# Kernel optimization log

Measured on AMD Instinct MI355X. Metric: run time of the kernel, lower is better.

Reference implementation:

```python
import jax, jax.numpy as jnp
import numpy as np

FFT_SIZE = 16384

def setup_inputs() -> dict:
    key = jax.random.key(0)
    k1, k2 = jax.random.split(key)
    u = jax.random.normal(k1, (8, 1024, 8192), dtype=jnp.float32)
    k = jax.random.normal(k2, (1024, 8192), dtype=jnp.float32)
    return {"u": u, "k": k}

def reference(u, k):
    # Faithful port of PyTorchFFTConv.forward with fft_size=FFT_SIZE.
    L = u.shape[-1]
    u_f32 = u.astype(jnp.float32)
    k_f32 = k.astype(jnp.float32)
    if k_f32.ndim == 2:
        k_f32 = k_f32[None]  # (1, H, L) -> broadcasts over batch
    u_fft = jnp.fft.rfft(u_f32, n=FFT_SIZE, axis=-1)   # (B, H, fft/2+1) complex64
    k_fft = jnp.fft.rfft(k_f32, n=FFT_SIZE, axis=-1)
    y_fft = u_fft * k_fft / FFT_SIZE
    # irfft with norm='forward' (no 1/n on inverse) combined with the /fft_s above
    # yields the standard circular convolution, matching the torch code exactly.
    y = jnp.fft.irfft(y_fft, n=FFT_SIZE, axis=-1, norm='forward')
    return y[..., :L].astype(jnp.float32)
```

## Files before the change

### kernel.cpp

```cpp
#include <hip/hip_runtime.h>

#define NFFT 16384
#define LSIG 8192
#define NH   1024
#define NTH  512
#define LDSC (NFFT + ((NFFT >> 5) << 1))

__device__ __forceinline__ int PADC(int i) { return i + ((i >> 5) << 1); }
__device__ __forceinline__ int PADI(int i) { return i + (i >> 5); }

struct cplx { float x, y; };
__device__ __forceinline__ cplx cadd(cplx a, cplx b){ return {a.x+b.x, a.y+b.y}; }
__device__ __forceinline__ cplx csub(cplx a, cplx b){ return {a.x-b.x, a.y-b.y}; }
__device__ __forceinline__ cplx cmul(cplx a, cplx b){ return {a.x*b.x - a.y*b.y, a.x*b.y + a.y*b.x}; }

template<int V> struct ic { static constexpr int value = V; };
template<int Start, int End, typename F>
__device__ __forceinline__ void cfor(F&& f) {
  if constexpr (Start < End) { f(ic<Start>{}); cfor<Start+1, End>(static_cast<F&&>(f)); }
}

constexpr float W32C32[32] = {
  1.0f, 0.9807852804f, 0.9238795325f, 0.8314696123f,
  0.7071067812f, 0.5555702330f, 0.3826834324f, 0.1950903220f,
  0.0f, -0.1950903220f, -0.3826834324f, -0.5555702330f,
  -0.7071067812f, -0.8314696123f, -0.9238795325f, -0.9807852804f,
  -1.0f, -0.9807852804f, -0.9238795325f, -0.8314696123f,
  -0.7071067812f, -0.5555702330f, -0.3826834324f, -0.1950903220f,
  0.0f, 0.1950903220f, 0.3826834324f, 0.5555702330f,
  0.7071067812f, 0.8314696123f, 0.9238795325f, 0.9807852804f };
constexpr float W32S32[32] = {
  0.0f, 0.1950903220f, 0.3826834324f, 0.5555702330f,
  0.7071067812f, 0.8314696123f, 0.9238795325f, 0.9807852804f,
  1.0f, 0.9807852804f, 0.9238795325f, 0.8314696123f,
  0.7071067812f, 0.5555702330f, 0.3826834324f, 0.1950903220f,
  0.0f, -0.1950903220f, -0.3826834324f, -0.5555702330f,
  -0.7071067812f, -0.8314696123f, -0.9238795325f, -0.9807852804f,
  -1.0f, -0.9807852804f, -0.9238795325f, -0.8314696123f,
  -0.7071067812f, -0.5555702330f, -0.3826834324f, -0.1950903220f };
constexpr int BR3[8] = {0,4,2,6,1,5,3,7};

template<int KK, bool INV>
__device__ __forceinline__ cplx twid(cplx d) {
  constexpr int K = KK & 31;
  if constexpr (K == 0)       return d;
  else if constexpr (K == 8)  { if constexpr (INV) return cplx{-d.y, d.x}; else return cplx{d.y, -d.x}; }
  else if constexpr (K == 16) return cplx{-d.x, -d.y};
  else if constexpr (K == 24) { if constexpr (INV) return cplx{d.y, -d.x}; else return cplx{-d.y, d.x}; }
  else {
    constexpr float c = W32C32[K];
    constexpr float s = INV ? W32S32[K] : -W32S32[K];
    return cmul(d, cplx{c, s});
  }
}

template<int N, int SP, bool INV>
__device__ __forceinline__ void fft_pass(cplx* z) {
  #pragma unroll
  for (int b = 0; b < N; b += 2*SP) {
    cfor<0, SP>([&](auto rc){
      constexpr int r = decltype(rc)::value;
      constexpr int KK = r * (16 / SP);
      if constexpr (!INV) {
        cplx u = z[b+r], v = z[b+r+SP];
        z[b+r]    = cadd(u, v);
        z[b+r+SP] = twid<KK,false>(csub(u, v));
      } else {
        cplx t0 = z[b+r], t1 = z[b+r+SP];
        cplx w = twid<KK,true>(t1);
        z[b+r]    = cadd(t0, w);
        z[b+r+SP] = csub(t0, w);
      }
    });
  }
}

template<int N, bool INV>
__device__ __forceinline__ void fft_regs(cplx* z) {
  if constexpr (!INV) {
    if constexpr (N >= 32) fft_pass<N,16,false>(z);
    if constexpr (N >= 16) fft_pass<N, 8,false>(z);
    if constexpr (N >=  8) fft_pass<N, 4,false>(z);
    if constexpr (N >=  4) fft_pass<N, 2,false>(z);
    fft_pass<N,1,false>(z);
  } else {
    fft_pass<N,1,true>(z);
    if constexpr (N >=  4) fft_pass<N, 2,true>(z);
    if constexpr (N >=  8) fft_pass<N, 4,true>(z);
    if constexpr (N >= 16) fft_pass<N, 8,true>(z);
    if constexpr (N >= 32) fft_pass<N,16,true>(z);
  }
}

template<int S, bool INV>
__device__ __forceinline__ void stage8p(float2* sz, int tid) {
  const float ang1 = (INV ? 2.0f : -2.0f) * 3.14159265358979f / (float)(8 * S);
  #pragma unroll 1
  for (int it = 0; it < 2; ++it) {
    int pp = tid + it * NTH;
    int bf = 2 * pp;
    int q = bf / S;
    int r = bf - q * S;
    int base = q * (8 * S) + r;
    float ta = ang1 * (float)r;
    float tb = ang1 * (float)(r + 1);
    cplx w1a = {__cosf(ta), __sinf(ta)};
    cplx w1b = {__cosf(tb), __sinf(tb)};
    cplx wa[8], wb[8];
    wa[1]=w1a; wa[2]=cmul(w1a,w1a); wa[3]=cmul(wa[2],w1a); wa[4]=cmul(wa[2],wa[2]);
    wa[5]=cmul(wa[4],wa[1]); wa[6]=cmul(wa[4],wa[2]); wa[7]=cmul(wa[4],wa[3]);
    wb[1]=w1b; wb[2]=cmul(w1b,w1b); wb[3]=cmul(wb[2],w1b); wb[4]=cmul(wb[2],wb[2]);
    wb[5]=cmul(wb[4],wb[1]); wb[6]=cmul(wb[4],wb[2]); wb[7]=cmul(wb[4],wb[3]);

    cplx A[8], B[8];
    if constexpr (!INV) {
      cfor<0,8>([&](auto jc){ constexpr int j = decltype(jc)::value;
        float4 v = *reinterpret_cast<const float4*>(&sz[PADC(base + j*S)]);
        A[j] = {v.x, v.y}; B[j] = {v.z, v.w}; });
      fft_regs<8,false>(A);
      fft_regs<8,false>(B);
      cfor<0,8>([&](auto pc){ constexpr int p = decltype(pc)::value;
        constexpr int m = BR3[p];
        cplx oa, ob;
        if constexpr (m == 0) { oa = A[p]; ob = B[p]; }
        else { oa = cmul(A[p], wa[m]); ob = cmul(B[p], wb[m]); }
        *reinterpret_cast<float4*>(&sz[PADC(base + m*S)]) = make_float4(oa.x, oa.y, ob.x, ob.y); });
    } else {
      cfor<0,8>([&](auto pc){ constexpr int p = decltype(pc)::value;
        constexpr int m = BR3[p];
        float4 v = *reinterpret_cast<const float4*>(&sz[PADC(base + m*S)]);
        if constexpr (m == 0) { A[p] = {v.x, v.y}; B[p] = {v.z, v.w}; }
        else { A[p] = cmul(cplx{v.x, v.y}, wa[m]); B[p] = cmul(cplx{v.z, v.w}, wb[m]); } });
      fft_regs<8,true>(A);
      fft_regs<8,true>(B);
      cfor<0,8>([&](auto jc){ constexpr int j = decltype(jc)::value;
        *reinterpret_cast<float4*>(&sz[PADC(base + j*S)]) = make_float4(A[j].x, A[j].y, B[j].x, B[j].y); });
    }
  }
}

template<bool INV>
__device__ __forceinline__ void stage8_s4p(float2* sz, int tid) {
  cfor<0,2>([&](auto rrc){
    constexpr int r0 = decltype(rrc)::value * 2;
    int base = tid * 32 + r0;
    cplx A[8], B[8];
    if constexpr (!INV) {
      cfor<0,8>([&](auto jc){ constexpr int j = decltype(jc)::value;
        float4 v = *reinterpret_cast<const float4*>(&sz[PADC(base + j*4)]);
        A[j] = {v.x, v.y}; B[j] = {v.z, v.w}; });
      fft_regs<8,false>(A);
      fft_regs<8,false>(B);
      cfor<0,8>([&](auto pc){ constexpr int p = decltype(pc)::value;
        constexpr int m = BR3[p];
        cplx oa = twid<r0*m, false>(A[p]);
        cplx ob = twid<(r0+1)*m, false>(B[p]);
        *reinterpret_cast<float4*>(&sz[PADC(base + m*4)]) = make_float4(oa.x, oa.y, ob.x, ob.y); });
    } else {
      cfor<0,8>([&](auto pc){ constexpr int p = decltype(pc)::value;
        constexpr int m = BR3[p];
        float4 v = *reinterpret_cast<const float4*>(&sz[PADC(base + m*4)]);
        A[p] = twid<r0*m, true>(cplx{v.x, v.y});
        B[p] = twid<(r0+1)*m, true>(cplx{v.z, v.w}); });
      fft_regs<8,true>(A);
      fft_regs<8,true>(B);
      cfor<0,8>([&](auto jc){ constexpr int j = decltype(jc)::value;
        *reinterpret_cast<float4*>(&sz[PADC(base + j*4)]) = make_float4(A[j].x, A[j].y, B[j].x, B[j].y); });
    }
  });
}

__global__ __launch_bounds__(NTH)
void kfft_kernel(const float* __restrict__ kin, float2* __restrict__ kh) {
  __shared__ __align__(16) float2 sz[LDSC];
  const int tid = threadIdx.x;
  const int h = blockIdx.x;
  const float* krow = kin + (size_t)h * LSIG;
  const float ang1 = -2.0f * 3.14159265358979f / (float)NFFT;

  #pragma unroll 1
  for (int it = 0; it < 2; ++it) {
    int base = 2*tid + 1024*it;
    cplx A[8], B[8];
    cfor<0,4>([&](auto jc){ constexpr int j = decltype(jc)::value;
      float2 kr = *reinterpret_cast<const float2*>(krow + base + j*2048);
      A[j] = {kr.x, 0.f}; B[j] = {kr.y, 0.f}; });
    cfor<0,4>([&](auto jc){ constexpr int j = decltype(jc)::value;
      A[j+4] = twid<4*j,false>(A[j]);
      B[j+4] = twid<4*j,false>(B[j]); });
    fft_pass<8,2,false>(A); fft_pass<8,1,false>(A);
    fft_pass<8,2,false>(B); fft_pass<8,1,false>(B);
    float ta = ang1 * (float)base, tb = ang1 * (float)(base + 1);
    cplx w1a = {__cosf(ta), __sinf(ta)};
    cplx w1b = {__cosf(tb), __sinf(tb)};
    cplx wa[8], wb[8];
    wa[1]=w1a; wa[2]=cmul(w1a,w1a); wa[3]=cmul(wa[2],w1a); wa[4]=cmul(wa[2],wa[2]);
    wa[5]=cmul(wa[4],wa[1]); wa[6]=cmul(wa[4],wa[2]); wa[7]=cmul(wa[4],wa[3]);
    wb[1]=w1b; wb[2]=cmul(w1b,w1b); wb[3]=cmul(wb[2],w1b); wb[4]=cmul(wb[2],wb[2]);
    wb[5]=cmul(wb[4],wb[1]); wb[6]=cmul(wb[4],wb[2]); wb[7]=cmul(wb[4],wb[3]);
    cfor<0,8>([&](auto pc){ constexpr int p = decltype(pc)::value;
      constexpr int m = BR3[p];
      cplx oa, ob;
      if constexpr (m == 0) { oa = A[p]; ob = B[p]; }
      else { oa = cmul(A[p], wa[m]); ob = cmul(B[p], wb[m]); }
      *reinterpret_cast<float4*>(&sz[PADC(base + m*2048)]) = make_float4(oa.x, oa.y, ob.x, ob.y); });
  }
  __syncthreads();
  stage8p< 256,false>(sz, tid); __syncthreads();
  stage8p<  32,false>(sz, tid); __syncthreads();
  stage8_s4p<false>(sz, tid);

  const float scl = 1.0f / (float)NFFT;
  float2* row = kh + (size_t)h * NFFT;
  #pragma unroll
  for (int s = 0; s < 8; ++s) {
    int ci = 32*tid + 4*s;
    float4 f0 = *reinterpret_cast<const float4*>(&sz[PADC(ci)]);
    float4 f1 = *reinterpret_cast<const float4*>(&sz[PADC(ci + 2)]);
    cplx z[4] = { {f0.x, f0.y}, {f0.z, f0.w}, {f1.x, f1.y}, {f1.z, f1.w} };
    fft_regs<4,false>(z);
    *reinterpret_cast<float4*>(row + ci)     = make_float4(z[0].x*scl, z[0].y*scl, z[1].x*scl, z[1].y*scl);
    *reinterpret_cast<float4*>(row + ci + 2) = make_float4(z[2].x*scl, z[2].y*scl, z[3].x*scl, z[3].y*scl);
  }
}

__global__ __launch_bounds__(NTH)
void conv_kernel(const float* __restrict__ u, const float2* __restrict__ kh,
                 float* __restrict__ out) {
  __shared__ __align__(16) float2 sz[LDSC];
  const int tid = threadIdx.x;
  const int bid = blockIdx.x;
  const int h  = bid >> 2;
  const int pr = bid & 3;

  const float* u0 = u + ((size_t)(2*pr) * NH + h) * LSIG;
  const float* u1 = u0 + (size_t)NH * LSIG;
  float* o0 = out + ((size_t)(2*pr) * NH + h) * LSIG;
  float* o1 = o0 + (size_t)NH * LSIG;

  {
    const float ang1 = -2.0f * 3.14159265358979f / (float)NFFT;
    #pragma unroll 1
    for (int it = 0; it < 2; ++it) {
      int base = 2*tid + 1024*it;
      cplx A[8], B[8];
      cfor<0,4>([&](auto jc){ constexpr int j = decltype(jc)::value;
        float2 a2 = *reinterpret_cast<const float2*>(u0 + base + j*2048);
        float2 b2 = *reinterpret_cast<const float2*>(u1 + base + j*2048);
        A[j] = {a2.x, b2.x}; B[j] = {a2.y, b2.y}; });
      cfor<0,4>([&](auto jc){ constexpr int j = decltype(jc)::value;
        A[j+4] = twid<4*j,false>(A[j]);
        B[j+4] = twid<4*j,false>(B[j]); });
      fft_pass<8,2,false>(A); fft_pass<8,1,false>(A);
      fft_pass<8,2,false>(B); fft_pass<8,1,false>(B);
      float ta = ang1 * (float)base, tb = ang1 * (float)(base + 1);
      cplx w1a = {__cosf(ta), __sinf(ta)};
      cplx w1b = {__cosf(tb), __sinf(tb)};
      cplx wa[8], wb[8];
      wa[1]=w1a; wa[2]=cmul(w1a,w1a); wa[3]=cmul(wa[2],w1a); wa[4]=cmul(wa[2],wa[2]);
      wa[5]=cmul(wa[4],wa[1]); wa[6]=cmul(wa[4],wa[2]); wa[7]=cmul(wa[4],wa[3]);
      wb[1]=w1b; wb[2]=cmul(w1b,w1b); wb[3]=cmul(wb[2],w1b); wb[4]=cmul(wb[2],wb[2]);
      wb[5]=cmul(wb[4],wb[1]); wb[6]=cmul(wb[4],wb[2]); wb[7]=cmul(wb[4],wb[3]);
      cfor<0,8>([&](auto pc){ constexpr int p = decltype(pc)::value;
        constexpr int m = BR3[p];
        cplx oa, ob;
        if constexpr (m == 0) { oa = A[p]; ob = B[p]; }
        else { oa = cmul(A[p], wa[m]); ob = cmul(B[p], wb[m]); }
        *reinterpret_cast<float4*>(&sz[PADC(base + m*2048)]) = make_float4(oa.x, oa.y, ob.x, ob.y); });
    }
  }
  __syncthreads();
  stage8p< 256,false>(sz, tid); __syncthreads();
  stage8p<  32,false>(sz, tid); __syncthreads();

  stage8_s4p<false>(sz, tid);
  {
    const float2* krow = kh + (size_t)h * NFFT;
    #pragma unroll
    for (int s = 0; s < 8; ++s) {
      int ci = 32*tid + 4*s;
      float4 f0 = *reinterpret_cast<const float4*>(&sz[PADC(ci)]);
      float4 f1 = *reinterpret_cast<const float4*>(&sz[PADC(ci + 2)]);
      cplx z[4] = { {f0.x, f0.y}, {f0.z, f0.w}, {f1.x, f1.y}, {f1.z, f1.w} };
      fft_regs<4,false>(z);
      float4 k0 = *reinterpret_cast<const float4*>(krow + ci);
      float4 k1 = *reinterpret_cast<const float4*>(krow + ci + 2);
      z[0] = cmul(z[0], cplx{k0.x, k0.y});
      z[1] = cmul(z[1], cplx{k0.z, k0.w});
      z[2] = cmul(z[2], cplx{k1.x, k1.y});
      z[3] = cmul(z[3], cplx{k1.z, k1.w});
      fft_regs<4,true>(z);
      *reinterpret_cast<float4*>(&sz[PADC(ci)])     = make_float4(z[0].x, z[0].y, z[1].x, z[1].y);
      *reinterpret_cast<float4*>(&sz[PADC(ci + 2)]) = make_float4(z[2].x, z[2].y, z[3].x, z[3].y);
    }
  }
  stage8_s4p<true>(sz, tid);
  __syncthreads();
  stage8p<  32,true>(sz, tid); __syncthreads();
  stage8p< 256,true>(sz, tid); __syncthreads();

  {
    const float ang1 = 2.0f * 3.14159265358979f / (float)NFFT;
    #pragma unroll 1
    for (int it = 0; it < 2; ++it) {
      int base = 2*tid + 1024*it;
      float ta = ang1 * (float)base, tb = ang1 * (float)(base + 1);
      cplx w1a = {__cosf(ta), __sinf(ta)};
      cplx w1b = {__cosf(tb), __sinf(tb)};
      cplx wa[8], wb[8];
      wa[1]=w1a; wa[2]=cmul(w1a,w1a); wa[3]=cmul(wa[2],w1a); wa[4]=cmul(wa[2],wa[2]);
      wa[5]=cmul(wa[4],wa[1]); wa[6]=cmul(wa[4],wa[2]); wa[7]=cmul(wa[4],wa[3]);
      wb[1]=w1b; wb[2]=cmul(w1b,w1b); wb[3]=cmul(wb[2],w1b); wb[4]=cmul(wb[2],wb[2]);
      wb[5]=cmul(wb[4],wb[1]); wb[6]=cmul(wb[4],wb[2]); wb[7]=cmul(wb[4],wb[3]);
      cplx A[8], B[8];
      cfor<0,8>([&](auto pc){ constexpr int p = decltype(pc)::value;
        constexpr int m = BR3[p];
        float4 v = *reinterpret_cast<const float4*>(&sz[PADC(base + m*2048)]);
        if constexpr (m == 0) { A[p] = {v.x, v.y}; B[p] = {v.z, v.w}; }
        else { A[p] = cmul(cplx{v.x, v.y}, wa[m]); B[p] = cmul(cplx{v.z, v.w}, wb[m]); } });
      fft_pass<8,1,true>(A); fft_pass<8,2,true>(A);
      fft_pass<8,1,true>(B); fft_pass<8,2,true>(B);
      cfor<0,4>([&](auto rc){ constexpr int r = decltype(rc)::value;
        cplx yA = cadd(A[r], twid<4*r,true>(A[r+4]));
        cplx yB = cadd(B[r], twid<4*r,true>(B[r+4]));
        *reinterpret_cast<float2*>(o0 + base + r*2048) = make_float2(yA.x, yB.x);
        *reinterpret_cast<float2*>(o1 + base + r*2048) = make_float2(yA.y, yB.y); });
    }
  }
}

template<int S, bool INV>
__device__ __forceinline__ void stage8f(float* sre, float* sim, int tid) {
  const float ang1 = (INV ? 2.0f : -2.0f) * 3.14159265358979f / (float)(8 * S);
  #pragma unroll
  for (int it = 0; it < (NFFT/8)/NTH; ++it) {
    int bf = tid + it * NTH;
    int q = bf / S;
    int r = bf - q * S;
    int base = q * (8 * S) + r;
    float t = ang1 * (float)r;
    cplx w1 = {__cosf(t), __sinf(t)};
    cplx wp[8];
    wp[0] = {1.0f, 0.0f};
    wp[1] = w1; wp[2] = cmul(w1, w1); wp[3] = cmul(wp[2], w1); wp[4] = cmul(wp[2], wp[2]);
    wp[5] = cmul(wp[4], wp[1]); wp[6] = cmul(wp[4], wp[2]); wp[7] = cmul(wp[4], wp[3]);
    cplx a[8];
    if constexpr (!INV) {
      cfor<0,8>([&](auto jc){ constexpr int j = decltype(jc)::value;
        int idx = PADI(base + j*S); a[j] = {sre[idx], sim[idx]}; });
      fft_regs<8,false>(a);
      cfor<0,8>([&](auto pc){ constexpr int p = decltype(pc)::value;
        constexpr int m = BR3[p];
        cplx o; if constexpr (m == 0) o = a[p]; else o = cmul(a[p], wp[m]);
        int idx = PADI(base + m*S); sre[idx] = o.x; sim[idx] = o.y; });
    } else {
      cfor<0,8>([&](auto pc){ constexpr int p = decltype(pc)::value;
        constexpr int m = BR3[p];
        int idx = PADI(base + m*S); cplx v = {sre[idx], sim[idx]};
        if constexpr (m == 0) a[p] = v; else a[p] = cmul(v, wp[m]); });
      fft_regs<8,true>(a);
      cfor<0,8>([&](auto jc){ constexpr int j = decltype(jc)::value;
        int idx = PADI(base + j*S); sre[idx] = a[j].x; sim[idx] = a[j].y; });
    }
  }
}

template<bool INV>
__device__ __forceinline__ void stage8_s4f(float* sre, float* sim, int tid) {
  cfor<0,4>([&](auto rc){
    constexpr int r = decltype(rc)::value;
    int base = tid * 32 + r;
    cplx a[8];
    if constexpr (!INV) {
      cfor<0,8>([&](auto jc){ constexpr int j = decltype(jc)::value;
        int idx = PADI(base + j*4); a[j] = {sre[idx], sim[idx]}; });
      fft_regs<8,false>(a);
      cfor<0,8>([&](auto pc){ constexpr int p = decltype(pc)::value;
        constexpr int m = BR3[p];
        cplx o = twid<r*m, false>(a[p]);
        int idx = PADI(base + m*4); sre[idx] = o.x; sim[idx] = o.y; });
    } else {
      cfor<0,8>([&](auto pc){ constexpr int p = decltype(pc)::value;
        constexpr int m = BR3[p];
        int idx = PADI(base + m*4); cplx v = {sre[idx], sim[idx]};
        a[p] = twid<r*m, true>(v); });
      fft_regs<8,true>(a);
      cfor<0,8>([&](auto jc){ constexpr int j = decltype(jc)::value;
        int idx = PADI(base + j*4); sre[idx] = a[j].x; sim[idx] = a[j].y; });
    }
  });
}

__global__ __launch_bounds__(NTH)
void fftconv_fallback(const float* __restrict__ u, const float* __restrict__ kin,
                      float* __restrict__ out) {
  __shared__ float sre[NFFT + (NFFT >> 5)];
  __shared__ float sim[NFFT + (NFFT >> 5)];
  const int tid = threadIdx.x;
  const int bid = blockIdx.x;
  const int h  = bid >> 2;
  const int pr = bid & 3;

  const float* krow = kin + (size_t)h * LSIG;
  #pragma unroll
  for (int c = 0; c < 4; ++c) {
    int i0 = (c * NTH + tid) * 4;
    float4 v = *reinterpret_cast<const float4*>(krow + i0);
    int p0 = PADI(i0);
    sre[p0+0]=v.x; sre[p0+1]=v.y; sre[p0+2]=v.z; sre[p0+3]=v.w;
    sim[p0+0]=0.f; sim[p0+1]=0.f; sim[p0+2]=0.f; sim[p0+3]=0.f;
    int p1 = PADI(i0 + LSIG);
    sre[p1+0]=0.f; sre[p1+1]=0.f; sre[p1+2]=0.f; sre[p1+3]=0.f;
    sim[p1+0]=0.f; sim[p1+1]=0.f; sim[p1+2]=0.f; sim[p1+3]=0.f;
  }
  __syncthreads();
  stage8f<2048,false>(sre, sim, tid); __syncthreads();
  stage8f< 256,false>(sre, sim, tid); __syncthreads();
  stage8f<  32,false>(sre, sim, tid); __syncthreads();
  stage8_s4f<false>(sre, sim, tid);   __syncthreads();

  cplx kq[4][4];
  cplx kq2[4][4];
  const float scl = 1.0f / (float)NFFT;
  #pragma unroll
  for (int s = 0; s < 8; ++s) {
    int m = tid + NTH * s;
    int p = PADI(4 * m);
    cplx z[4] = { {sre[p+0], sim[p+0]}, {sre[p+1], sim[p+1]},
                  {sre[p+2], sim[p+2]}, {sre[p+3], sim[p+3]} };
    fft_regs<4,false>(z);
    #pragma unroll
    for (int e = 0; e < 4; ++e) {
      cplx v = {z[e].x*scl, z[e].y*scl};
      if (s < 4) kq[s][e] = v; else kq2[s-4][e] = v;
    }
  }
  __syncthreads();

  const float* u0 = u + ((size_t)(2*pr) * NH + h) * LSIG;
  const float* u1 = u0 + (size_t)NH * LSIG;
  #pragma unroll
  for (int c = 0; c < 4; ++c) {
    int i0 = (c * NTH + tid) * 4;
    float4 a = *reinterpret_cast<const float4*>(u0 + i0);
    float4 b = *reinterpret_cast<const float4*>(u1 + i0);
    int p0 = PADI(i0);
    sre[p0+0]=a.x; sre[p0+1]=a.y; sre[p0+2]=a.z; sre[p0+3]=a.w;
    sim[p0+0]=b.x; sim[p0+1]=b.y; sim[p0+2]=b.z; sim[p0+3]=b.w;
    int p1 = PADI(i0 + LSIG);
    sre[p1+0]=0.f; sre[p1+1]=0.f; sre[p1+2]=0.f; sre[p1+3]=0.f;
    sim[p1+0]=0.f; sim[p1+1]=0.f; sim[p1+2]=0.f; sim[p1+3]=0.f;
  }
  __syncthreads();
  stage8f<2048,false>(sre, sim, tid); __syncthreads();
  stage8f< 256,false>(sre, sim, tid); __syncthreads();
  stage8f<  32,false>(sre, sim, tid); __syncthreads();
  stage8_s4f<false>(sre, sim, tid);   __syncthreads();

  #pragma unroll
  for (int s = 0; s < 8; ++s) {
    int m = tid + NTH * s;
    int p = PADI(4 * m);
    cplx z[4] = { {sre[p+0], sim[p+0]}, {sre[p+1], sim[p+1]},
                  {sre[p+2], sim[p+2]}, {sre[p+3], sim[p+3]} };
    fft_regs<4,false>(z);
    #pragma unroll
    for (int e = 0; e < 4; ++e) z[e] = cmul(z[e], (s<4) ? kq[s][e] : kq2[s-4][e]);
    fft_regs<4,true>(z);
    #pragma unroll
    for (int e = 0; e < 4; ++e) { sre[p+e] = z[e].x; sim[p+e] = z[e].y; }
  }
  __syncthreads();
  stage8_s4f<true>(sre, sim, tid);   __syncthreads();
  stage8f<  32,true>(sre, sim, tid); __syncthreads();
  stage8f< 256,true>(sre, sim, tid); __syncthreads();
  stage8f<2048,true>(sre, sim, tid); __syncthreads();

  float* o0 = out + ((size_t)(2*pr) * NH + h) * LSIG;
  float* o1 = o0 + (size_t)NH * LSIG;
  #pragma unroll
  for (int c = 0; c < 4; ++c) {
    int i0 = (c * NTH + tid) * 4;
    int p0 = PADI(i0);
    float4 a = {sre[p0], sre[p0+1], sre[p0+2], sre[p0+3]};
    float4 b = {sim[p0], sim[p0+1], sim[p0+2], sim[p0+3]};
    *reinterpret_cast<float4*>(o0 + i0) = a;
    *reinterpret_cast<float4*>(o1 + i0) = b;
  }
}

extern "C" void kernel_launch(void* const* d_in, const int* in_sizes, int n_in,
                              void* d_out, int out_size, void* d_ws, size_t ws_size,
                              hipStream_t stream) {
  (void)in_sizes; (void)n_in; (void)out_size;
  const float* u = (const float*)d_in[0];
  const float* k = (const float*)d_in[1];
  float* out = (float*)d_out;
  const size_t need = (size_t)NH * NFFT * sizeof(float2);
  if (ws_size >= need) {
    hipLaunchKernelGGL(kfft_kernel, dim3(NH),   dim3(NTH), 0, stream, k, (float2*)d_ws);
    hipLaunchKernelGGL(conv_kernel, dim3(4096), dim3(NTH), 0, stream, u, (const float2*)d_ws, out);
  } else {
    hipLaunchKernelGGL(fftconv_fallback, dim3(4096), dim3(NTH), 0, stream, u, k, out);
  }
}
```

Baseline: 431.0 us.

## Remap stride-32 FFT stage to warp-local data and coalesce spectrum layout

Replaces the stride-32 radix-8 stage with a variant whose thread-to-butterfly mapping keeps each 256-element group inside a single 64-thread wavefront. This lets the barriers between that stage and the neighbouring stride-4 stage be dropped in both forward and inverse passes. The kernel spectrum is also stored and read in a permuted order (s*2048 + 4*tid) so global accesses are coalesced across threads. The risk is correctness: dropping barriers relies on wavefront-synchronous LDS behaviour, and the spectrum layout must match exactly between the producer and consumer kernels.

```diff
diff --git a/kernel.cpp b/kernel.cpp
--- a/kernel.cpp
+++ b/kernel.cpp
@@ -140,6 +140,53 @@
 }
 
 template<bool INV>
+__device__ __forceinline__ void stage8p32w(float2* sz, int tid) {
+  const float ang1 = (INV ? 2.0f : -2.0f) * 3.14159265358979f / 256.0f;
+  #pragma unroll 1
+  for (int it = 0; it < 2; ++it) {
+    int pp = 128 * (tid >> 6) + (tid & 63) + 64 * it;
+    int bf = 2 * pp;
+    int q = bf >> 5;
+    int r = bf & 31;
+    int base = q * 256 + r;
+    float ta = ang1 * (float)r;
+    float tb = ang1 * (float)(r + 1);
+    cplx w1a = {__cosf(ta), __sinf(ta)};
+    cplx w1b = {__cosf(tb), __sinf(tb)};
+    cplx wa[8], wb[8];
+    wa[1]=w1a; wa[2]=cmul(w1a,w1a); wa[3]=cmul(wa[2],w1a); wa[4]=cmul(wa[2],wa[2]);
+    wa[5]=cmul(wa[4],wa[1]); wa[6]=cmul(wa[4],wa[2]); wa[7]=cmul(wa[4],wa[3]);
+    wb[1]=w1b; wb[2]=cmul(w1b,w1b); wb[3]=cmul(wb[2],w1b); wb[4]=cmul(wb[2],wb[2]);
+    wb[5]=cmul(wb[4],wb[1]); wb[6]=cmul(wb[4],wb[2]); wb[7]=cmul(wb[4],wb[3]);
+
+    cplx A[8], B[8];
+    if constexpr (!INV) {
+      cfor<0,8>([&](auto jc){ constexpr int j = decltype(jc)::value;
+        float4 v = *reinterpret_cast<const float4*>(&sz[PADC(base + j*32)]);
+        A[j] = {v.x, v.y}; B[j] = {v.z, v.w}; });
+      fft_regs<8,false>(A);
+      fft_regs<8,false>(B);
+      cfor<0,8>([&](auto pc){ constexpr int p = decltype(pc)::value;
+        constexpr int m = BR3[p];
+        cplx oa, ob;
+        if constexpr (m == 0) { oa = A[p]; ob = B[p]; }
+        else { oa = cmul(A[p], wa[m]); ob = cmul(B[p], wb[m]); }
+        *reinterpret_cast<float4*>(&sz[PADC(base + m*32)]) = make_float4(oa.x, oa.y, ob.x, ob.y); });
+    } else {
+      cfor<0,8>([&](auto pc){ constexpr int p = decltype(pc)::value;
+        constexpr int m = BR3[p];
+        float4 v = *reinterpret_cast<const float4*>(&sz[PADC(base + m*32)]);
+        if constexpr (m == 0) { A[p] = {v.x, v.y}; B[p] = {v.z, v.w}; }
+        else { A[p] = cmul(cplx{v.x, v.y}, wa[m]); B[p] = cmul(cplx{v.z, v.w}, wb[m]); } });
+      fft_regs<8,true>(A);
+      fft_regs<8,true>(B);
+      cfor<0,8>([&](auto jc){ constexpr int j = decltype(jc)::value;
+        *reinterpret_cast<float4*>(&sz[PADC(base + j*32)]) = make_float4(A[j].x, A[j].y, B[j].x, B[j].y); });
+    }
+  }
+}
+
+template<bool INV>
 __device__ __forceinline__ void stage8_s4p(float2* sz, int tid) {
   cfor<0,2>([&](auto rrc){
     constexpr int r0 = decltype(rrc)::value * 2;
@@ -161,7 +208,8 @@
         constexpr int m = BR3[p];
         float4 v = *reinterpret_cast<const float4*>(&sz[PADC(base + m*4)]);
         A[p] = twid<r0*m, true>(cplx{v.x, v.y});
-        B[p] = twid<(r0+1)*m, true>(cplx{v.z, v.w}); });
+        B[p] = twid<(r0+1)*m, true>(cplx{v.z, v.w});
+      });
       fft_regs<8,true>(A);
       fft_regs<8,true>(B);
       cfor<0,8>([&](auto jc){ constexpr int j = decltype(jc)::value;
@@ -207,7 +255,7 @@
   }
   __syncthreads();
   stage8p< 256,false>(sz, tid); __syncthreads();
-  stage8p<  32,false>(sz, tid); __syncthreads();
+  stage8p32w<false>(sz, tid);
   stage8_s4p<false>(sz, tid);
 
   const float scl = 1.0f / (float)NFFT;
@@ -219,8 +267,9 @@
     float4 f1 = *reinterpret_cast<const float4*>(&sz[PADC(ci + 2)]);
     cplx z[4] = { {f0.x, f0.y}, {f0.z, f0.w}, {f1.x, f1.y}, {f1.z, f1.w} };
     fft_regs<4,false>(z);
-    *reinterpret_cast<float4*>(row + ci)     = make_float4(z[0].x*scl, z[0].y*scl, z[1].x*scl, z[1].y*scl);
-    *reinterpret_cast<float4*>(row + ci + 2) = make_float4(z[2].x*scl, z[2].y*scl, z[3].x*scl, z[3].y*scl);
+    float2* dst = row + s*2048 + 4*tid;
+    *reinterpret_cast<float4*>(dst)     = make_float4(z[0].x*scl, z[0].y*scl, z[1].x*scl, z[1].y*scl);
+    *reinterpret_cast<float4*>(dst + 2) = make_float4(z[2].x*scl, z[2].y*scl, z[3].x*scl, z[3].y*scl);
   }
 }
 
@@ -271,11 +320,11 @@
   }
   __syncthreads();
   stage8p< 256,false>(sz, tid); __syncthreads();
-  stage8p<  32,false>(sz, tid); __syncthreads();
-
+
+  stage8p32w<false>(sz, tid);
   stage8_s4p<false>(sz, tid);
   {
-    const float2* krow = kh + (size_t)h * NFFT;
+    const float2* kp = kh + (size_t)h * NFFT;
     #pragma unroll
     for (int s = 0; s < 8; ++s) {
       int ci = 32*tid + 4*s;
@@ -283,8 +332,9 @@
       float4 f1 = *reinterpret_cast<const float4*>(&sz[PADC(ci + 2)]);
       cplx z[4] = { {f0.x, f0.y}, {f0.z, f0.w}, {f1.x, f1.y}, {f1.z, f1.w} };
       fft_regs<4,false>(z);
-      float4 k0 = *reinterpret_cast<const float4*>(krow + ci);
-      float4 k1 = *reinterpret_cast<const float4*>(krow + ci + 2);
+      const float2* kq = kp + s*2048 + 4*tid;
+      float4 k0 = *reinterpret_cast<const float4*>(kq);
+      float4 k1 = *reinterpret_cast<const float4*>(kq + 2);
       z[0] = cmul(z[0], cplx{k0.x, k0.y});
       z[1] = cmul(z[1], cplx{k0.z, k0.w});
       z[2] = cmul(z[2], cplx{k1.x, k1.y});
@@ -295,8 +345,9 @@
     }
   }
   stage8_s4p<true>(sz, tid);
-  __syncthreads();
-  stage8p<  32,true>(sz, tid); __syncthreads();
+  stage8p32w<true>(sz, tid);
+  __syncthreads();
+
   stage8p< 256,true>(sz, tid); __syncthreads();
 
   {
```

Measured after the change: 374.8 us. -13.0%, faster.
